# Kernel optimization log

Measured on AMD Instinct MI355X. Metric: run time of the kernel, lower is better.

Reference implementation:

```python
import jax, jax.numpy as jnp
import numpy as np

M, K, N, GROUP = 32, 8192, 28672, 128


def setup_inputs() -> dict:
    key = jax.random.key(0)
    k1, k2, k3, k4 = jax.random.split(key, 4)
    x = jax.random.normal(k1, (M, K), dtype=jnp.float16)
    # int32 words, each packing 8 consecutive int4 values along K
    qweight = jax.random.randint(k2, (K // 8, N), 0, 2147483647, dtype=jnp.int32)
    scales = (jax.random.uniform(k3, (K // GROUP, N), dtype=jnp.float32) * 0.01 + 0.001).astype(jnp.float16)
    bias = (jax.random.normal(k4, (N,), dtype=jnp.float32) * 0.02).astype(jnp.float16)
    return {"x": x, "qweight": qweight, "scales": scales, "bias": bias}


def reference(x, qweight, scales, bias):
    # Unpack 8 int4 nibbles per int32 word along K: (K//8, N) -> (K, N)
    K8, n = qweight.shape
    shifts = (jnp.arange(8, dtype=jnp.int32) * 4)[None, :, None]
    wq = ((qweight[:, None, :] >> shifts) & 15).reshape(K8 * 8, n)  # [K, N] in [0,15]
    # Dequant: zero-point fixed at 8 (pack() asserts zeros==8), per-group scales
    w = wq.astype(jnp.float16) - jnp.float16(8.0)
    g, gs = scales.shape[0], (K8 * 8) // scales.shape[0]
    w = (w.reshape(g, gs, n) * scales[:, None, :]).reshape(K8 * 8, n)  # [K, N] fp16
    return jnp.dot(x, w) + bias  # [M, N]
```

## Files before the change

kernel.cpp:

```cpp
#include <hip/hip_runtime.h>
#include <stdint.h>

#define K_DIM 8192
#define N_DIM 28672

typedef _Float16 half8 __attribute__((ext_vector_type(8)));
typedef _Float16 half2t __attribute__((ext_vector_type(2)));
typedef float f32x16 __attribute__((ext_vector_type(16)));

__global__ __launch_bounds__(256) void prep_x(const float* __restrict__ x,
                                              _Float16* __restrict__ xp) {
  int idx = blockIdx.x * 256 + threadIdx.x;
  int m  = idx & 31;
  int k8 = idx >> 5;
  const float* p = x + (size_t)m * K_DIM + (size_t)k8 * 8;
  float4 xa = *(const float4*)p;
  float4 xb = *(const float4*)(p + 4);
  half2t p0 = __builtin_bit_cast(half2t, __builtin_amdgcn_cvt_pkrtz(xa.x, xb.x));
  half2t p1 = __builtin_bit_cast(half2t, __builtin_amdgcn_cvt_pkrtz(xa.y, xb.y));
  half2t p2 = __builtin_bit_cast(half2t, __builtin_amdgcn_cvt_pkrtz(xa.z, xb.z));
  half2t p3 = __builtin_bit_cast(half2t, __builtin_amdgcn_cvt_pkrtz(xa.w, xb.w));
  half8 o;
  o[0] = p0[0]; o[1] = p0[1]; o[2] = p1[0]; o[3] = p1[1];
  o[4] = p2[0]; o[5] = p2[1]; o[6] = p3[0]; o[7] = p3[1];
  *(half8*)(xp + ((size_t)k8 * 32 + m) * 8) = o;
}

__global__ __launch_bounds__(256) void zero_out(float4* __restrict__ out) {
  out[(size_t)blockIdx.x * 256 + threadIdx.x] = float4{0.f, 0.f, 0.f, 0.f};
}

static __device__ __forceinline__ half8 dqs(uint32_t w, half2t sh) {
  const uint32_t M4 = 0x000F000Fu, E = 0x64006400u;
  half2t off; off[0] = (_Float16)(-1032.0f); off[1] = (_Float16)(-1032.0f);
  half2t v0 = (__builtin_bit_cast(half2t, ( w        & M4) | E) + off) * sh;
  half2t v1 = (__builtin_bit_cast(half2t, ((w >> 4)  & M4) | E) + off) * sh;
  half2t v2 = (__builtin_bit_cast(half2t, ((w >> 8)  & M4) | E) + off) * sh;
  half2t v3 = (__builtin_bit_cast(half2t, ((w >> 12) & M4) | E) + off) * sh;
  half8 r;
  r[0] = v0[0]; r[1] = v0[1]; r[2] = v1[0]; r[3] = v1[1];
  r[4] = v2[0]; r[5] = v2[1]; r[6] = v3[0]; r[7] = v3[1];
  return r;
}

static __device__ __forceinline__ void gl_lds16(const void* g, void* l) {
  __builtin_amdgcn_global_load_lds(
      (const __attribute__((address_space(1))) uint32_t*)g,
      (__attribute__((address_space(3))) uint32_t*)l, 16, 0, 0);
}

static __device__ __forceinline__ void waitcnt_vm(int n) {
  switch (n) {
    case 0: __builtin_amdgcn_s_waitcnt(0x0F70); break;
    case 4: __builtin_amdgcn_s_waitcnt(0x0F74); break;
    default: __builtin_amdgcn_s_waitcnt(0x0F78); break;
  }
}

__global__ __launch_bounds__(256, 4) void qgemm(
    const uint32_t* __restrict__ q, const float* __restrict__ scales,
    const float* __restrict__ bias, const _Float16* __restrict__ xp,
    float* __restrict__ out) {
  __shared__ __attribute__((aligned(16))) char smem[3 * 16384];
  const int tid  = threadIdx.x;
  const int w    = tid >> 6;
  const int lane = tid & 63;
  const int h    = lane >> 5;
  const int nl   = lane & 31;
  const int bid  = blockIdx.x;
  const int kblk = bid & 7;
  const int col0 = (bid >> 3) << 7;
  const int wr0  = kblk << 7;
  const int colw = col0 + (w << 5);

  half2t sh[8];
#pragma unroll
  for (int g = 0; g < 8; g++) {
    float s = scales[(size_t)(kblk * 8 + g) * N_DIM + colw + nl];
    sh[g] = __builtin_bit_cast(half2t, __builtin_amdgcn_cvt_pkrtz(s, s));
  }

  const char* xb = (const char*)xp;
  auto stage = [&](int g) {
    char* A = smem + (g % 3) * 16384;
    char* Q = A + 8192;
    size_t ga = (size_t)(wr0 + 16 * g) * 512 + (size_t)w * 2048 + (size_t)lane * 16;
#pragma unroll
    for (int j = 0; j < 2; j++)
      gl_lds16(xb + ga + j * 1024, A + w * 2048 + j * 1024);
#pragma unroll
    for (int j = 0; j < 2; j++) {
      int row = wr0 + 16 * g + 4 * w + 2 * j + h;
      gl_lds16(q + (size_t)row * N_DIM + col0 + nl * 4, Q + (4 * w + 2 * j) * 512);
    }
  };

  f32x16 acc;
#pragma unroll
  for (int j = 0; j < 16; j++) acc[j] = 0.0f;

  stage(0); stage(1); stage(2);

#pragma unroll
  for (int g = 0; g < 8; g++) {
    waitcnt_vm(g <= 5 ? 8 : (g == 6 ? 4 : 0));
    __builtin_amdgcn_s_barrier();
    const char* A = smem + (g % 3) * 16384;
    const char* Q = A + 8192;
    half2t s = sh[g];
#pragma unroll
    for (int i = 0; i < 8; i++) {
      half8 af = *(const half8*)(A + (size_t)((2 * i + h) * 32 + nl) * 16);
      uint32_t wq = *(const uint32_t*)(Q + (2 * i + h) * 512 + (w * 32 + nl) * 4);
      acc = __builtin_amdgcn_mfma_f32_32x32x16_f16(af, dqs(wq, s), acc, 0, 0, 0);
    }
    __builtin_amdgcn_s_barrier();
    if (g + 3 < 8) stage(g + 3);
  }

  float bs = (kblk == 0) ? bias[colw + nl] : 0.0f;
#pragma unroll
  for (int j = 0; j < 16; j++) {
    int row = (j & 3) + ((j >> 2) << 3) + (h << 2);
    unsafeAtomicAdd(&out[(size_t)row * N_DIM + colw + nl], acc[j] + bs);
  }
}

extern "C" void kernel_launch(void* const* d_in, const int* in_sizes, int n_in,
                              void* d_out, int out_size, void* d_ws, size_t ws_size,
                              hipStream_t stream) {
  const float*    xf      = (const float*)d_in[0];
  const uint32_t* qweight = (const uint32_t*)d_in[1];
  const float*    scales  = (const float*)d_in[2];
  const float*    bias    = (const float*)d_in[3];
  float*          out     = (float*)d_out;
  _Float16*       xp      = (_Float16*)d_ws;

  zero_out<<<dim3(896), dim3(256), 0, stream>>>((float4*)out);
  prep_x<<<dim3(128), dim3(256), 0, stream>>>(xf, xp);
  qgemm<<<dim3((N_DIM / 128) * 8), dim3(256), 0, stream>>>(qweight, scales, bias, xp, out);
}
```

Measured before the change: 190.2 us.

## Load int4 weights directly into registers and reorder block-to-tile mapping

Quantized weights now go from global memory straight into registers through inline-asm global_load_dword with a scalar base, instead of being staged in LDS. LDS holds only the activation tiles, which halves shared memory per block, and the pipeline moves from three stages issued ahead to two, with the prefetch issued right after the barrier. That removes the second barrier per step. Block indexing becomes k-block-major, so blocks that run at the same time cover different column tiles of the same K slice. The risks are that per-lane dword loads coalesce less well than 16-byte LDS loads, and that hand-written waitcnt values must match the exact order in which loads are issued.

```diff
diff --git a/kernel.cpp b/kernel.cpp
--- a/kernel.cpp
+++ b/kernel.cpp
@@ -3,6 +3,7 @@
 
 #define K_DIM 8192
 #define N_DIM 28672
+#define NCT   (N_DIM / 128)
 
 typedef _Float16 half8 __attribute__((ext_vector_type(8)));
 typedef _Float16 half2t __attribute__((ext_vector_type(2)));
@@ -49,27 +50,23 @@
       (__attribute__((address_space(3))) uint32_t*)l, 16, 0, 0);
 }
 
-static __device__ __forceinline__ void waitcnt_vm(int n) {
-  switch (n) {
-    case 0: __builtin_amdgcn_s_waitcnt(0x0F70); break;
-    case 4: __builtin_amdgcn_s_waitcnt(0x0F74); break;
-    default: __builtin_amdgcn_s_waitcnt(0x0F78); break;
-  }
-}
+static __device__ __forceinline__ void waitcnt_vm10() { __builtin_amdgcn_s_waitcnt(0x0F7A); }
+static __device__ __forceinline__ void waitcnt_vm0()  { __builtin_amdgcn_s_waitcnt(0x0F70); }
 
 __global__ __launch_bounds__(256, 4) void qgemm(
     const uint32_t* __restrict__ q, const float* __restrict__ scales,
     const float* __restrict__ bias, const _Float16* __restrict__ xp,
     float* __restrict__ out) {
-  __shared__ __attribute__((aligned(16))) char smem[3 * 16384];
+  __shared__ __attribute__((aligned(16))) char smem[3 * 8192];
   const int tid  = threadIdx.x;
   const int w    = tid >> 6;
   const int lane = tid & 63;
   const int h    = lane >> 5;
   const int nl   = lane & 31;
   const int bid  = blockIdx.x;
-  const int kblk = bid & 7;
-  const int col0 = (bid >> 3) << 7;
+  const int kblk = bid / NCT;
+  const int ct   = bid - kblk * NCT;
+  const int col0 = ct << 7;
   const int wr0  = kblk << 7;
   const int colw = col0 + (w << 5);
 
@@ -79,43 +76,52 @@
     float s = scales[(size_t)(kblk * 8 + g) * N_DIM + colw + nl];
     sh[g] = __builtin_bit_cast(half2t, __builtin_amdgcn_cvt_pkrtz(s, s));
   }
+  __builtin_amdgcn_sched_barrier(0);
 
+  const uint64_t sb = (uint64_t)(uintptr_t)q +
+                      ((uint64_t)wr0 * N_DIM + (uint64_t)col0) * 4u;
+  const uint32_t vbase = (uint32_t)(((h * N_DIM) + (w << 5) + nl) * 4);
   const char* xb = (const char*)xp;
-  auto stage = [&](int g) {
-    char* A = smem + (g % 3) * 16384;
-    char* Q = A + 8192;
-    size_t ga = (size_t)(wr0 + 16 * g) * 512 + (size_t)w * 2048 + (size_t)lane * 16;
+
+  uint32_t qr[3][8];
+
+  auto qload = [&](int gg) {
+#pragma unroll
+    for (int i = 0; i < 8; i++) {
+      uint32_t vo = vbase + (uint32_t)(8 * gg + i) * (uint32_t)(2 * N_DIM * 4);
+      asm volatile("global_load_dword %0, %1, %2"
+                   : "=v"(qr[gg % 3][i])
+                   : "v"(vo), "s"(sb));
+    }
+  };
+  auto stageA = [&](int gg) {
+    char* A = smem + (gg % 3) * 8192;
+    size_t ga = (size_t)(wr0 + 16 * gg) * 512 + (size_t)w * 2048 + (size_t)lane * 16;
 #pragma unroll
     for (int j = 0; j < 2; j++)
       gl_lds16(xb + ga + j * 1024, A + w * 2048 + j * 1024);
-#pragma unroll
-    for (int j = 0; j < 2; j++) {
-      int row = wr0 + 16 * g + 4 * w + 2 * j + h;
-      gl_lds16(q + (size_t)row * N_DIM + col0 + nl * 4, Q + (4 * w + 2 * j) * 512);
-    }
   };
 
   f32x16 acc;
 #pragma unroll
   for (int j = 0; j < 16; j++) acc[j] = 0.0f;
 
-  stage(0); stage(1); stage(2);
+  qload(0); stageA(0); qload(1); stageA(1);
 
 #pragma unroll
   for (int g = 0; g < 8; g++) {
-    waitcnt_vm(g <= 5 ? 8 : (g == 6 ? 4 : 0));
+    if (g < 7) waitcnt_vm10(); else waitcnt_vm0();
     __builtin_amdgcn_s_barrier();
-    const char* A = smem + (g % 3) * 16384;
-    const char* Q = A + 8192;
+    __builtin_amdgcn_sched_barrier(0);
+    if (g + 2 < 8) { qload(g + 2); stageA(g + 2); }
+    const char* A = smem + (g % 3) * 8192;
     half2t s = sh[g];
 #pragma unroll
     for (int i = 0; i < 8; i++) {
-      half8 af = *(const half8*)(A + (size_t)((2 * i + h) * 32 + nl) * 16);
-      uint32_t wq = *(const uint32_t*)(Q + (2 * i + h) * 512 + (w * 32 + nl) * 4);
-      acc = __builtin_amdgcn_mfma_f32_32x32x16_f16(af, dqs(wq, s), acc, 0, 0, 0);
+      half8 af = *(const half8*)(A + ((2 * i + h) * 32 + nl) * 16);
+      acc = __builtin_amdgcn_mfma_f32_32x32x16_f16(af, dqs(qr[g % 3][i], s),
+                                                   acc, 0, 0, 0);
     }
-    __builtin_amdgcn_s_barrier();
-    if (g + 3 < 8) stage(g + 3);
   }
 
   float bs = (kblk == 0) ? bias[colw + nl] : 0.0f;
@@ -138,5 +144,5 @@
 
   zero_out<<<dim3(896), dim3(256), 0, stream>>>((float4*)out);
   prep_x<<<dim3(128), dim3(256), 0, stream>>>(xf, xp);
-  qgemm<<<dim3((N_DIM / 128) * 8), dim3(256), 0, stream>>>(qweight, scales, bias, xp, out);
+  qgemm<<<dim3(NCT * 8), dim3(256), 0, stream>>>(qweight, scales, bias, xp, out);
 }
```

New measurement: 187.4 us. Within noise of the previous version (-1.5%).
